# Performance work log

Measured on AMD Instinct MI355X. Metric: run time of the kernel, lower is better.

The kernel has to match this reference:

```python
import jax, jax.numpy as jnp
import numpy as np

B, IDF, CDF, IH, IW, SL = 32, 768, 768, 32, 32, 128

def setup_inputs() -> dict:
    key = jax.random.key(0)
    k1, k2, k3, k4 = jax.random.split(key, 4)
    inp = jax.random.normal(k1, (B, IDF, IH, IW), dtype=jnp.float32)
    ctx = jax.random.normal(k2, (B, CDF, SL), dtype=jnp.float32)
    mask = jax.random.randint(k3, (B, SL), 0, 2, dtype=jnp.int32)
    # 1x1 conv with no bias == matmul weight [idf, cdf]
    w_conv = jax.random.normal(k4, (IDF, CDF), dtype=jnp.float32) * 0.02
    return {"input": inp, "context": ctx, "mask": mask, "w_conv": w_conv}

def reference(input, context, mask, w_conv):
    b, idf, ih, iw = input.shape
    queryL = ih * iw
    sourceL = context.shape[2]
    # target: b x idf x queryL
    target = input.reshape(b, idf, queryL)
    # 1x1 conv projection of context: b x idf x sourceL
    sourceT = jnp.einsum('oc,bcs->bos', w_conv, context)
    # attention logits: b x queryL x sourceL (targetT @ sourceT)
    attn = jnp.einsum('biq,bis->bqs', target, sourceT)
    attn = attn + mask[:, None, :].astype(attn.dtype) * (-10000.0)
    attn = jax.nn.softmax(attn, axis=-1)  # softmax over sourceL
    # weighted context: sourceT @ attn^T -> b x idf x queryL
    weightedContext = jnp.einsum('bis,bqs->biq', sourceT, attn).reshape(b, idf, ih, iw)
    attn_out = jnp.transpose(attn, (0, 2, 1)).reshape(b, sourceL, ih, iw)
    return weightedContext, attn_out
```

## Files before the change

kernel.cpp:

```cpp
#include <hip/hip_runtime.h>

#define NB  32
#define IDF 768
#define SLN 128
#define QLN 1024
#define NT2 12

typedef _Float16 v8hf __attribute__((ext_vector_type(8)));
typedef _Float16 v4hf __attribute__((ext_vector_type(4)));
typedef float    v4f  __attribute__((ext_vector_type(4)));

#define MFMAH __builtin_amdgcn_mfma_f32_16x16x32_f16

__device__ __forceinline__ void gload16(const void* g, void* l) {
  __builtin_amdgcn_global_load_lds(
      (const __attribute__((address_space(1))) void*)g,
      (__attribute__((address_space(3))) void*)l, 16, 0, 0);
}

__device__ __forceinline__ void lbar() {
  asm volatile("s_waitcnt lgkmcnt(0)" ::: "memory");
  __builtin_amdgcn_sched_barrier(0);
  __builtin_amdgcn_s_barrier();
  __builtin_amdgcn_sched_barrier(0);
}

__global__ __launch_bounds__(256) void prep_k(const float* __restrict__ W,
                                              const float* __restrict__ ctx,
                                              _Float16* __restrict__ Wf,
                                              _Float16* __restrict__ cTf) {
  const int bid = blockIdx.x, t = threadIdx.x;
  __shared__ float tl[64][133];
  if (bid < 576) {
    int idx = bid * 1024 + t * 4;
    float4 v = *(const float4*)(W + idx);
    v4hf h;
    h[0] = (_Float16)v.x;
    h[1] = (_Float16)v.y;
    h[2] = (_Float16)v.z;
    h[3] = (_Float16)v.w;
    *(v4hf*)(Wf + idx) = h;
    return;
  }
  const int cid = bid - 576;
  const int b = cid / 12, c0 = (cid % 12) * 64;
#pragma unroll
  for (int j = 0; j < 8; ++j) {
    int u = j * 256 + t;
    int c = u >> 5, s4 = (u & 31) * 4;
    *(float4*)&tl[c][s4] =
        *(const float4*)(ctx + ((size_t)b * IDF + c0 + c) * SLN + s4);
  }
  __syncthreads();
#pragma unroll
  for (int j = 0; j < 8; ++j) {
    int u = j * 256 + t;
    int s = u >> 4, c4 = (u & 15) * 4;
    v4hf h;
#pragma unroll
    for (int e = 0; e < 4; ++e) h[e] = (_Float16)tl[c4 + e][s];
    *(v4hf*)(cTf + ((size_t)b * SLN + s) * IDF + c0 + c4) = h;
  }
}

__global__ __launch_bounds__(256) void proj_k(const _Float16* __restrict__ cTf,
                                              const _Float16* __restrict__ Wf,
                                              _Float16* __restrict__ STf,
                                              _Float16* __restrict__ Shvf) {
  const int b = blockIdx.y, o0 = blockIdx.x * 32;
  const int t = threadIdx.x, w = t >> 6, lane = t & 63;
  const int lr = lane & 15, lg = lane >> 4;
  const int ws = w >> 1, wq = w & 1;
  __shared__ _Float16 AL[128][72];

  v4f acc[4];
#pragma unroll
  for (int fr = 0; fr < 4; ++fr) acc[fr] = (v4f){0.f, 0.f, 0.f, 0.f};

  const int ra = t >> 1;
  const int cb = (t & 1) * 4;
  const _Float16* pA = cTf + ((size_t)b * SLN + ra) * IDF + cb * 8;
  const size_t wOff = (size_t)(o0 + wq * 16 + lr) * IDF + lg * 8;

  uint4 aS0, aS1, aS2, aS3, bS0, bS1, bS2, bS3;
  v8hf wc0, wc1, wn0, wn1;
  aS0 = *(const uint4*)(pA);
  aS1 = *(const uint4*)(pA + 8);
  aS2 = *(const uint4*)(pA + 16);
  aS3 = *(const uint4*)(pA + 24);
  bS0 = *(const uint4*)(pA + 64);
  bS1 = *(const uint4*)(pA + 72);
  bS2 = *(const uint4*)(pA + 80);
  bS3 = *(const uint4*)(pA + 88);
  wc0 = *(const v8hf*)(Wf + wOff);
  wc1 = *(const v8hf*)(Wf + wOff + 32);

#define PROJ_BODY(S0, S1, S2, S3, IT)                                          \
  {                                                                            \
    lbar();                                                                    \
    *(uint4*)&AL[ra][(cb + 0) * 8] = S0;                                       \
    *(uint4*)&AL[ra][(cb + 1) * 8] = S1;                                       \
    *(uint4*)&AL[ra][(cb + 2) * 8] = S2;                                       \
    *(uint4*)&AL[ra][(cb + 3) * 8] = S3;                                       \
    if ((IT) + 2 < NT2) {                                                      \
      S0 = *(const uint4*)(pA + ((IT) + 2) * 64);                              \
      S1 = *(const uint4*)(pA + ((IT) + 2) * 64 + 8);                          \
      S2 = *(const uint4*)(pA + ((IT) + 2) * 64 + 16);                         \
      S3 = *(const uint4*)(pA + ((IT) + 2) * 64 + 24);                         \
    }                                                                          \
    if ((IT) + 1 < NT2) {                                                      \
      wn0 = *(const v8hf*)(Wf + wOff + ((IT) + 1) * 64);                       \
      wn1 = *(const v8hf*)(Wf + wOff + ((IT) + 1) * 64 + 32);                  \
    }                                                                          \
    lbar();                                                                    \
    _Pragma("unroll") for (int fr = 0; fr < 4; ++fr) {                         \
      const int r = ws * 64 + fr * 16 + lr;                                    \
      v8hf ah0 = *(const v8hf*)&AL[r][lg * 8];                                 \
      acc[fr] = MFMAH(ah0, wc0, acc[fr], 0, 0, 0);                             \
      v8hf ah1 = *(const v8hf*)&AL[r][32 + lg * 8];                            \
      acc[fr] = MFMAH(ah1, wc1, acc[fr], 0, 0, 0);                             \
    }                                                                          \
    wc0 = wn0;                                                                 \
    wc1 = wn1;                                                                 \
  }

  for (int it2 = 0; it2 < NT2 / 2; ++it2) {
    const int itE = it2 * 2;
    PROJ_BODY(aS0, aS1, aS2, aS3, itE);
    PROJ_BODY(bS0, bS1, bS2, bS3, itE + 1);
  }
#undef PROJ_BODY

  const int o = o0 + wq * 16 + lr;
#pragma unroll
  for (int fr = 0; fr < 4; ++fr) {
    v4hf hp;
#pragma unroll
    for (int r = 0; r < 4; ++r) {
      int s = ws * 64 + fr * 16 + lg * 4 + r;
      _Float16 h = (_Float16)acc[fr][r];
      STf[((size_t)b * SLN + s) * IDF + o] = h;
      hp[r] = h;
    }
    *(v4hf*)(Shvf + ((size_t)b * IDF + o) * SLN + ws * 64 + fr * 16 + lg * 4) =
        hp;
  }
}

__global__ __launch_bounds__(256, 4) void qkpv_k(const float* __restrict__ input,
                                                 const _Float16* __restrict__ STf,
                                                 const _Float16* __restrict__ Shvf,
                                                 const int* __restrict__ mask,
                                                 float* __restrict__ wc,
                                                 float* __restrict__ attn_out) {
  const int bid = blockIdx.x;
  const int nid = (bid & 7) * 64 + (bid >> 3);
  const int b = nid >> 4, q0 = (nid & 15) * 64;
  const int t = threadIdx.x, w = t >> 6, lane = t & 63;
  const int lr = lane & 15, lg = lane >> 4;

  __shared__ __align__(16) char lds[33280];
  float* const msk = (float*)(lds + 32768);
  char* const PLb = lds;

  if (t < SLN) msk[t] = -10000.0f * (float)mask[b * SLN + t];

  v4f acc[8];
#pragma unroll
  for (int fr = 0; fr < 8; ++fr) acc[fr] = (v4f){0.f, 0.f, 0.f, 0.f};

  const int rA = (lane >> 3);
  const int cpA = lane & 7;
  const _Float16* gA[4];
#pragma unroll
  for (int g = 0; g < 4; ++g) {
    const int row = w * 32 + g * 8 + rA;
    const int c = cpA ^ (row & 7);
    gA[g] = STf + ((size_t)b * SLN + row) * IDF + c * 8;
  }
  const int dA = w * 4096;

  const float* gB = input + (size_t)b * IDF * QLN + q0 + w * 16 + lr;

#pragma unroll
  for (int g = 0; g < 4; ++g) gload16(gA[g], lds + dA + g * 1024);
  v8hf aH[2], bH[2];
  float tmpB[2][8];
#pragma unroll
  for (int kk = 0; kk < 2; ++kk)
#pragma unroll
    for (int e = 0; e < 8; ++e)
      tmpB[kk][e] = gB[(size_t)(kk * 32 + lg * 8 + e) * QLN];
#pragma unroll
  for (int kk = 0; kk < 2; ++kk)
#pragma unroll
    for (int e = 0; e < 8; ++e) aH[kk][e] = (_Float16)tmpB[kk][e];
#pragma unroll
  for (int g = 0; g < 4; ++g) gload16(gA[g] + 64, lds + 16384 + dA + g * 1024);

#define QK_WIN(CUROFF, BC, BN, IT, VMC)                                        \
  {                                                                            \
    asm volatile("s_waitcnt vmcnt(" #VMC ")" ::: "memory");                    \
    __builtin_amdgcn_sched_barrier(0);                                         \
    __builtin_amdgcn_s_barrier();                                              \
    __builtin_amdgcn_sched_barrier(0);                                         \
    if ((IT) + 1 < NT2) {                                                      \
      _Pragma("unroll") for (int kk = 0; kk < 2; ++kk)                         \
          _Pragma("unroll") for (int e = 0; e < 8; ++e)                        \
          tmpB[kk][e] =                                                        \
              gB[(size_t)(((IT) + 1) * 64 + kk * 32 + lg * 8 + e) * QLN];      \
    }                                                                          \
    __builtin_amdgcn_sched_barrier(0);                                         \
    const char* Ab = lds + (CUROFF);                                           \
    __builtin_amdgcn_s_setprio(1);                                             \
    _Pragma("unroll") for (int fr = 0; fr < 8; ++fr) {                         \
      const int r = fr * 16 + lr;                                              \
      _Pragma("unroll") for (int kk = 0; kk < 2; ++kk) {                       \
        const int cc = (kk * 4 + lg) ^ (r & 7);                                \
        v8hf ah = *(const v8hf*)(Ab + r * 128 + cc * 16);                      \
        acc[fr] = MFMAH(ah, BC[kk], acc[fr], 0, 0, 0);                         \
      }                                                                        \
    }                                                                          \
    __builtin_amdgcn_s_setprio(0);                                             \
    __builtin_amdgcn_sched_barrier(0);                                         \
    if ((IT) + 1 < NT2) {                                                      \
      _Pragma("unroll") for (int kk = 0; kk < 2; ++kk)                         \
          _Pragma("unroll") for (int e = 0; e < 8; ++e)                        \
          BN[kk][e] = (_Float16)tmpB[kk][e];                                   \
    }                                                                          \
    asm volatile("s_waitcnt lgkmcnt(0)" ::: "memory");                         \
    __builtin_amdgcn_s_barrier();                                              \
    if ((IT) + 2 < NT2) {                                                      \
      _Pragma("unroll") for (int g = 0; g < 4; ++g)                            \
          gload16(gA[g] + (size_t)((IT) + 2) * 64,                             \
                  lds + (CUROFF) + dA + g * 1024);                             \
    }                                                                          \
  }

  for (int it2 = 0; it2 < 5; ++it2) {
    const int itE = it2 * 2;
    QK_WIN(0, aH, bH, itE, 4);
    QK_WIN(16384, bH, aH, itE + 1, 4);
  }
  QK_WIN(0, aH, bH, 10, 4);
  QK_WIN(16384, bH, aH, 11, 0);
#undef QK_WIN

  const int qh = w * 16 + lr;
  float mx = -3.0e38f;
#pragma unroll
  for (int fr = 0; fr < 8; ++fr)
#pragma unroll
    for (int r = 0; r < 4; ++r) {
      acc[fr][r] += msk[fr * 16 + lg * 4 + r];
      mx = fmaxf(mx, acc[fr][r]);
    }
  mx = fmaxf(mx, __shfl_xor(mx, 16));
  mx = fmaxf(mx, __shfl_xor(mx, 32));
  float sum = 0.f;
#pragma unroll
  for (int fr = 0; fr < 8; ++fr)
#pragma unroll
    for (int r = 0; r < 4; ++r) {
      float e = __expf(acc[fr][r] - mx);
      acc[fr][r] = e;
      sum += e;
    }
  sum += __shfl_xor(sum, 16);
  sum += __shfl_xor(sum, 32);
  const float inv = 1.0f / sum;
  const int q = q0 + qh;
#pragma unroll
  for (int fr = 0; fr < 8; ++fr) {
    v4hf hp;
#pragma unroll
    for (int r = 0; r < 4; ++r) {
      float p = acc[fr][r] * inv;
      attn_out[((size_t)b * SLN + fr * 16 + lg * 4 + r) * QLN + q] = p;
      hp[r] = (_Float16)p;
    }
    const int g = (fr * 2 + (lg >> 1)) ^ lr;
    *(v4hf*)(PLb + qh * 256 + g * 16 + (lg & 1) * 8) = hp;
  }
  __syncthreads();

  const int qfp = (w & 1) * 2;
  const int islab = (w >> 1) * 384;
  v8hf pa0v[4], pa1v[4];
#pragma unroll
  for (int kt = 0; kt < 4; ++kt) {
    const int g0 = (kt * 4 + lg) ^ lr;
    pa0v[kt] = *(const v8hf*)(PLb + (qfp * 16 + lr) * 256 + g0 * 16);
    pa1v[kt] = *(const v8hf*)(PLb + ((qfp + 1) * 16 + lr) * 256 + g0 * 16);
  }
  const _Float16* pShv = Shvf + ((size_t)b * IDF + islab + lr) * SLN + lg * 8;
  float* pWc = wc + ((size_t)b * IDF + islab + lr) * QLN + q0;
#pragma unroll 2
  for (int ifr = 0; ifr < 24; ++ifr) {
    v4f a0 = (v4f){0.f, 0.f, 0.f, 0.f};
    v4f a1 = (v4f){0.f, 0.f, 0.f, 0.f};
#pragma unroll
    for (int kt = 0; kt < 4; ++kt) {
      v8hf bb = *(const v8hf*)(pShv + (size_t)(ifr * 16) * SLN + kt * 32);
      a0 = MFMAH(pa0v[kt], bb, a0, 0, 0, 0);
      a1 = MFMAH(pa1v[kt], bb, a1, 0, 0, 0);
    }
    *(float4*)(pWc + (size_t)(ifr * 16) * QLN + qfp * 16 + lg * 4) =
        make_float4(a0[0], a0[1], a0[2], a0[3]);
    *(float4*)(pWc + (size_t)(ifr * 16) * QLN + (qfp + 1) * 16 + lg * 4) =
        make_float4(a1[0], a1[1], a1[2], a1[3]);
  }
}

extern "C" void kernel_launch(void* const* d_in, const int* in_sizes, int n_in,
                              void* d_out, int out_size, void* d_ws, size_t ws_size,
                              hipStream_t stream) {
  const float* input   = (const float*)d_in[0];
  const float* context = (const float*)d_in[1];
  const int*   mask    = (const int*)d_in[2];
  const float* w_conv  = (const float*)d_in[3];

  float* out      = (float*)d_out;
  float* wc       = out;
  float* attn_out = out + (size_t)NB * IDF * QLN;

  const size_t SE = (size_t)NB * SLN * IDF;
  _Float16* wsb = (_Float16*)d_ws;
  _Float16* STf  = wsb;
  _Float16* Shvf = STf + SE;
  _Float16* scr  = (_Float16*)wc;
  _Float16* cTf  = scr;
  _Float16* Wf   = cTf + SE;

  prep_k<<<960, 256, 0, stream>>>(w_conv, context, Wf, cTf);
  proj_k<<<dim3(24, NB), 256, 0, stream>>>(cTf, Wf, STf, Shvf);
  qkpv_k<<<512, 256, 0, stream>>>(input, STf, Shvf, mask, wc, attn_out);
}
```

Before: 78.07 us.

## Stage fp32 input tiles through LDS via async global_load_lds in QK loop

```diff
diff --git a/kernel.cpp b/kernel.cpp
--- a/kernel.cpp
+++ b/kernel.cpp
@@ -147,7 +147,7 @@
   }
 }
 
-__global__ __launch_bounds__(256, 4) void qkpv_k(const float* __restrict__ input,
+__global__ __launch_bounds__(256, 2) void qkpv_k(const float* __restrict__ input,
                                                  const _Float16* __restrict__ STf,
                                                  const _Float16* __restrict__ Shvf,
                                                  const int* __restrict__ mask,
@@ -159,8 +159,8 @@
   const int t = threadIdx.x, w = t >> 6, lane = t & 63;
   const int lr = lane & 15, lg = lane >> 4;
 
-  __shared__ __align__(16) char lds[33280];
-  float* const msk = (float*)(lds + 32768);
+  __shared__ __align__(16) char lds[66048];
+  float* const msk = (float*)(lds + 65536);
   char* const PLb = lds;
 
   if (t < SLN) msk[t] = -10000.0f * (float)mask[b * SLN + t];
@@ -169,81 +169,84 @@
 #pragma unroll
   for (int fr = 0; fr < 8; ++fr) acc[fr] = (v4f){0.f, 0.f, 0.f, 0.f};
 
-  const int rA = (lane >> 3);
+  const int rAl = (lane >> 3);
   const int cpA = lane & 7;
   const _Float16* gA[4];
 #pragma unroll
   for (int g = 0; g < 4; ++g) {
-    const int row = w * 32 + g * 8 + rA;
+    const int row = w * 32 + g * 8 + rAl;
     const int c = cpA ^ (row & 7);
     gA[g] = STf + ((size_t)b * SLN + row) * IDF + c * 8;
   }
   const int dA = w * 4096;
 
-  const float* gB = input + (size_t)b * IDF * QLN + q0 + w * 16 + lr;
+  const float* gBp[4];
+#pragma unroll
+  for (int g = 0; g < 4; ++g) {
+    const int row = w * 16 + g * 4 + (lane >> 4);
+    gBp[g] = input + ((size_t)b * IDF + row) * QLN + q0 +
+             4 * ((lane & 15) ^ (row & 15));
+  }
+  const int dB = w * 4096;
 
 #pragma unroll
   for (int g = 0; g < 4; ++g) gload16(gA[g], lds + dA + g * 1024);
-  v8hf aH[2], bH[2];
-  float tmpB[2][8];
-#pragma unroll
-  for (int kk = 0; kk < 2; ++kk)
-#pragma unroll
-    for (int e = 0; e < 8; ++e)
-      tmpB[kk][e] = gB[(size_t)(kk * 32 + lg * 8 + e) * QLN];
-#pragma unroll
-  for (int kk = 0; kk < 2; ++kk)
-#pragma unroll
-    for (int e = 0; e < 8; ++e) aH[kk][e] = (_Float16)tmpB[kk][e];
-#pragma unroll
-  for (int g = 0; g < 4; ++g) gload16(gA[g] + 64, lds + 16384 + dA + g * 1024);
-
-#define QK_WIN(CUROFF, BC, BN, IT, VMC)                                        \
+#pragma unroll
+  for (int g = 0; g < 4; ++g) gload16(gBp[g], lds + 16384 + dB + g * 1024);
+#pragma unroll
+  for (int g = 0; g < 4; ++g) gload16(gA[g] + 64, lds + 32768 + dA + g * 1024);
+#pragma unroll
+  for (int g = 0; g < 4; ++g)
+    gload16(gBp[g] + (size_t)64 * QLN, lds + 49152 + dB + g * 1024);
+
+  const int qc = w * 4 + (lr >> 2);
+  const int qw = lr & 3;
+
+#define QK_WIN(AOFF, BOFF, IT, VMC)                                            \
   {                                                                            \
     asm volatile("s_waitcnt vmcnt(" #VMC ")" ::: "memory");                    \
     __builtin_amdgcn_sched_barrier(0);                                         \
     __builtin_amdgcn_s_barrier();                                              \
     __builtin_amdgcn_sched_barrier(0);                                         \
-    if ((IT) + 1 < NT2) {                                                      \
-      _Pragma("unroll") for (int kk = 0; kk < 2; ++kk)                         \
-          _Pragma("unroll") for (int e = 0; e < 8; ++e)                        \
-          tmpB[kk][e] =                                                        \
-              gB[(size_t)(((IT) + 1) * 64 + kk * 32 + lg * 8 + e) * QLN];      \
-    }                                                                          \
-    __builtin_amdgcn_sched_barrier(0);                                         \
-    const char* Ab = lds + (CUROFF);                                           \
+    const char* Ab = lds + (AOFF);                                             \
+    const char* Bb = lds + (BOFF);                                             \
+    v8hf bh[2];                                                                \
+    _Pragma("unroll") for (int kk = 0; kk < 2; ++kk)                           \
+        _Pragma("unroll") for (int e = 0; e < 8; ++e) {                        \
+      const int row = kk * 32 + lg * 8 + e;                                    \
+      const int ch = qc ^ (row & 15);                                          \
+      float v = *(const float*)(Bb + row * 256 + ch * 16 + qw * 4);            \
+      bh[kk][e] = (_Float16)v;                                                 \
+    }                                                                          \
     __builtin_amdgcn_s_setprio(1);                                             \
     _Pragma("unroll") for (int fr = 0; fr < 8; ++fr) {                         \
       const int r = fr * 16 + lr;                                              \
       _Pragma("unroll") for (int kk = 0; kk < 2; ++kk) {                       \
         const int cc = (kk * 4 + lg) ^ (r & 7);                                \
         v8hf ah = *(const v8hf*)(Ab + r * 128 + cc * 16);                      \
-        acc[fr] = MFMAH(ah, BC[kk], acc[fr], 0, 0, 0);                         \
+        acc[fr] = MFMAH(ah, bh[kk], acc[fr], 0, 0, 0);                         \
       }                                                                        \
     }                                                                          \
     __builtin_amdgcn_s_setprio(0);                                             \
-    __builtin_amdgcn_sched_barrier(0);                                         \
-    if ((IT) + 1 < NT2) {                                                      \
-      _Pragma("unroll") for (int kk = 0; kk < 2; ++kk)                         \
-          _Pragma("unroll") for (int e = 0; e < 8; ++e)                        \
-          BN[kk][e] = (_Float16)tmpB[kk][e];                                   \
-    }                                                                          \
     asm volatile("s_waitcnt lgkmcnt(0)" ::: "memory");                         \
     __builtin_amdgcn_s_barrier();                                              \
     if ((IT) + 2 < NT2) {                                                      \
       _Pragma("unroll") for (int g = 0; g < 4; ++g)                            \
           gload16(gA[g] + (size_t)((IT) + 2) * 64,                             \
-                  lds + (CUROFF) + dA + g * 1024);                             \
+                  lds + (AOFF) + dA + g * 1024);                               \
+      _Pragma("unroll") for (int g = 0; g < 4; ++g)                            \
+          gload16(gBp[g] + (size_t)((IT) + 2) * 64 * QLN,                      \
+                  lds + (BOFF) + dB + g * 1024);                               \
     }                                                                          \
   }
 
   for (int it2 = 0; it2 < 5; ++it2) {
     const int itE = it2 * 2;
-    QK_WIN(0, aH, bH, itE, 4);
-    QK_WIN(16384, bH, aH, itE + 1, 4);
-  }
-  QK_WIN(0, aH, bH, 10, 4);
-  QK_WIN(16384, bH, aH, 11, 0);
+    QK_WIN(0, 16384, itE, 8);
+    QK_WIN(32768, 49152, itE + 1, 8);
+  }
+  QK_WIN(0, 16384, 10, 8);
+  QK_WIN(32768, 49152, 11, 0);
 #undef QK_WIN
 
   const int qh = w * 16 + lr;
```

Result: faster. 74.46 us (-4.6%).
